# Optimization experiments

Hardware: AMD Instinct MI355X
Metric: run time of the kernel (lower is better)

## Reference

```python
import jax, jax.numpy as jnp
import numpy as np

LAG = 168
HORIZON = 24
D = 6            # d_model = 1 feature + 5-dim position embedding
FF = 18          # dim_feedforward
NL = 3           # num encoder layers
B = 8192
EPS = 1e-5


def setup_inputs() -> dict:
    key = jax.random.key(0)
    ks = jax.random.split(key, 16)
    s = 0.1
    return {
        "input": jax.random.normal(ks[0], (B, LAG), dtype=jnp.float32),
        "pos_emb": jax.random.normal(ks[1], (LAG, 5), dtype=jnp.float32) * s,
        "in_proj_w": jax.random.normal(ks[2], (NL, 3 * D, D), dtype=jnp.float32) * s,
        "in_proj_b": jax.random.normal(ks[3], (NL, 3 * D), dtype=jnp.float32) * s,
        "out_w": jax.random.normal(ks[4], (NL, D, D), dtype=jnp.float32) * s,
        "out_b": jax.random.normal(ks[5], (NL, D), dtype=jnp.float32) * s,
        "ln1_g": jnp.ones((NL, D), dtype=jnp.float32),
        "ln1_b": jnp.zeros((NL, D), dtype=jnp.float32),
        "lin1_w": jax.random.normal(ks[6], (NL, FF, D), dtype=jnp.float32) * s,
        "lin1_b": jax.random.normal(ks[7], (NL, FF), dtype=jnp.float32) * s,
        "lin2_w": jax.random.normal(ks[8], (NL, D, FF), dtype=jnp.float32) * s,
        "lin2_b": jax.random.normal(ks[9], (NL, D), dtype=jnp.float32) * s,
        "ln2_g": jnp.ones((NL, D), dtype=jnp.float32),
        "ln2_b": jnp.zeros((NL, D), dtype=jnp.float32),
        "head_w": jax.random.normal(ks[10], (HORIZON, D * LAG), dtype=jnp.float32) * s,
        "head_b": jax.random.normal(ks[11], (HORIZON,), dtype=jnp.float32) * s,
    }


def _layer_norm(x, g, b):
    m = jnp.mean(x, axis=-1, keepdims=True)
    v = jnp.mean((x - m) ** 2, axis=-1, keepdims=True)
    return (x - m) * jax.lax.rsqrt(v + EPS) * g + b


def reference(input, pos_emb, in_proj_w, in_proj_b, out_w, out_b,
              ln1_g, ln1_b, lin1_w, lin1_b, lin2_w, lin2_b,
              ln2_g, ln2_b, head_w, head_b):
    Bsz, L = input.shape
    # embed positions and concat with raw feature -> [B, L, 6]
    x = jnp.concatenate(
        [input[..., None], jnp.broadcast_to(pos_emb[None], (Bsz, L, 5))], axis=2)

    h = x
    scale = 1.0 / jnp.sqrt(jnp.float32(D))
    for i in range(NL):  # post-norm TransformerEncoderLayer (PyTorch default)
        qkv = jnp.einsum("bld,ed->ble", h, in_proj_w[i]) + in_proj_b[i]  # [B,L,18]
        q, k, v = jnp.split(qkv, 3, axis=-1)  # each [B,L,6], single head
        scores = jnp.einsum("bqd,bkd->bqk", q, k) * scale
        attn = jax.nn.softmax(scores, axis=-1)
        o = jnp.einsum("bqk,bkd->bqd", attn, v)
        o = jnp.einsum("bld,ed->ble", o, out_w[i]) + out_b[i]
        h = _layer_norm(h + o, ln1_g[i], ln1_b[i])
        f = jax.nn.relu(jnp.einsum("bld,fd->blf", h, lin1_w[i]) + lin1_b[i])
        f = jnp.einsum("blf,df->bld", f, lin2_w[i]) + lin2_b[i]
        h = _layer_norm(h + f, ln2_g[i], ln2_b[i])

    h = jax.nn.relu(h + x)              # residual from embedded input + relu
    h = h.reshape(Bsz, L * D)           # flatten
    return h @ head_w.T + head_b        # [B, HORIZON]
```

## Files before the change

kernel.cpp:

```cpp
#include <hip/hip_runtime.h>
#include <math.h>

#define LAG 168
#define HOR 24
#define DM 6
#define FFD 18
#define NL 3
#define LNEPS 1e-5f

typedef unsigned int u32;
typedef float f32x4 __attribute__((ext_vector_type(4)));
typedef float f32x16 __attribute__((ext_vector_type(16)));
typedef short s16x8 __attribute__((ext_vector_type(8)));
typedef __bf16 bfx2 __attribute__((ext_vector_type(2)));

#define VT    0
#define PP    800
#define OOH   2752
#define HEADS 0
#define LDSW  2144

__device__ __forceinline__ u32 pkbf(float a, float b) {
    bfx2 t; t[0] = (__bf16)a; t[1] = (__bf16)b;
    return __builtin_bit_cast(u32, t);
}
__device__ __forceinline__ s16x8 mk8(u32 a, u32 b, u32 c, u32 d) {
    uint4 u; u.x = a; u.y = b; u.z = c; u.w = d;
    return __builtin_bit_cast(s16x8, u);
}
__device__ __forceinline__ float b2f(unsigned short h) {
    u32 u = ((u32)h) << 16; return __builtin_bit_cast(float, u);
}
__device__ __forceinline__ void ln6(const float* r, const float* g, const float* bb, float* outv) {
    float m = (r[0]+r[1]+r[2]+r[3]+r[4]+r[5]) * (1.0f/6.0f);
    float v = 0.f;
#pragma unroll
    for (int d = 0; d < DM; ++d) { float t = r[d]-m; v += t*t; }
    v *= (1.0f/6.0f);
    float rs = __builtin_amdgcn_rsqf(v + LNEPS);
#pragma unroll
    for (int d = 0; d < DM; ++d) outv[d] = (r[d]-m)*rs*g[d] + bb[d];
}

__global__ __launch_bounds__(64, 4) void tfenc_kernel(
    const float* __restrict__ input, const float* __restrict__ pos_emb,
    const float* __restrict__ ipw, const float* __restrict__ ipb,
    const float* __restrict__ ow,  const float* __restrict__ obp,
    const float* __restrict__ l1g, const float* __restrict__ l1b,
    const float* __restrict__ f1w, const float* __restrict__ f1b,
    const float* __restrict__ f2w, const float* __restrict__ f2b,
    const float* __restrict__ l2g, const float* __restrict__ l2b,
    const float* __restrict__ hw,  const float* __restrict__ hb,
    float* __restrict__ out)
{
    __shared__ __align__(16) float lds[LDSW];
    __bf16* ldsh = (__bf16*)lds;
    u32*    ldsu = (u32*)lds;

    const int L = threadIdx.x;
    const int b = blockIdx.x;

    lds[VT + 700 + L] = 0.f;
    if (L < 36) lds[VT + 700 + 64 + L] = 0.f;
    {
        __bf16 one = (__bf16)1.0f;
        ldsh[6*200 + L] = one;
        ldsh[6*200 + 64 + L] = one;
        ldsh[6*200 + 128 + L] = one;
    }

    float hv[3][DM], xv[3][DM];
#pragma unroll
    for (int i = 0; i < 3; ++i) {
        int r = L + 64*i;
        bool real = (r < LAG);
        xv[i][0] = real ? input[(size_t)b*LAG + r] : 0.f;
#pragma unroll
        for (int j = 0; j < 5; ++j)
            xv[i][1+j] = real ? pos_emb[r*5 + j] : 0.f;
#pragma unroll
        for (int d = 0; d < DM; ++d) hv[i][d] = xv[i][d];
    }

    const float cQ = 0.5889116917845058f;
    const u32 himask = (L & 32) ? 0u : ~0u;
    const int permA = 4*(L & 31);
    const int permB = permA + 128;

#pragma unroll 1
    for (int il = 0; il < NL; ++il) {
        const float* Wip = ipw + il*3*DM*DM;
        const float* bip = ipb + il*3*DM;
        const float* Wo  = ow  + il*DM*DM;
        const float* bo  = obp + il*DM;
        const float* g1  = l1g + il*DM;    const float* c1 = l1b + il*DM;
        const float* W1  = f1w + il*FFD*DM; const float* bb1 = f1b + il*FFD;
        const float* W2  = f2w + il*DM*FFD; const float* bb2 = f2b + il*DM;
        const float* g2  = l2g + il*DM;    const float* c2 = l2b + il*DM;

        u32 qp[3][3], kp[3][3];
#pragma unroll
        for (int i = 0; i < 3; ++i) {
            int r = L + 64*i;
            float qv[6], kv[6], vv[6];
#pragma unroll
            for (int e = 0; e < 18; ++e) {
                float a = bip[e];
#pragma unroll
                for (int d = 0; d < DM; ++d) a += hv[i][d]*Wip[e*DM+d];
                if (e < 6) qv[e] = a*cQ;
                else if (e < 12) kv[e-6] = a;
                else vv[e-12] = a;
            }
            qp[i][0]=pkbf(qv[0],qv[1]); qp[i][1]=pkbf(qv[2],qv[3]); qp[i][2]=pkbf(qv[4],qv[5]);
            kp[i][0]=pkbf(kv[0],kv[1]); kp[i][1]=pkbf(kv[2],kv[3]); kp[i][2]=pkbf(kv[4],kv[5]);
#pragma unroll
            for (int d = 0; d < DM; ++d)
                ldsh[d*200 + r] = (__bf16)vv[d];
        }

        s16x8 kf[6];
#pragma unroll
        for (int kt = 0; kt < 6; ++kt) {
            int adr = (kt & 1) ? permB : permA;
            int sl = kt >> 1;
            u32 w0 = ((u32)__builtin_amdgcn_ds_bpermute(adr, (int)kp[sl][0])) & himask;
            u32 w1 = ((u32)__builtin_amdgcn_ds_bpermute(adr, (int)kp[sl][1])) & himask;
            u32 w2 = ((u32)__builtin_amdgcn_ds_bpermute(adr, (int)kp[sl][2])) & himask;
            kf[kt] = mk8(w0, w1, w2, 0u);
        }
        s16x8 vf[6];
        {
            int d = L & 15;
            int vrow = d < 7 ? d : 7;
            const u32* vb = ldsu + (VT + vrow*100 + (L >> 4)*4);
#pragma unroll
            for (int kc = 0; kc < 6; ++kc)
                vf[kc] = __builtin_bit_cast(s16x8, *(const uint4*)(vb + kc*16));
        }

        const int wrbase = PP + (L & 31)*18 + 2*(L >> 5);
        const int rdbase = PP + (L & 15)*18 + 4*(L >> 4);

#pragma unroll
        for (int qt = 0; qt < 6; ++qt) {
            int adr = (qt & 1) ? permB : permA;
            int sl = qt >> 1;
            u32 u0 = ((u32)__builtin_amdgcn_ds_bpermute(adr, (int)qp[sl][0])) & himask;
            u32 u1 = ((u32)__builtin_amdgcn_ds_bpermute(adr, (int)qp[sl][1])) & himask;
            u32 u2 = ((u32)__builtin_amdgcn_ds_bpermute(adr, (int)qp[sl][2])) & himask;
            s16x8 qf = mk8(u0, u1, u2, 0u);
            f32x4 acc0 = {0.f,0.f,0.f,0.f};
            f32x4 acc1 = {0.f,0.f,0.f,0.f};
#pragma unroll
            for (int kt = 0; kt < 6; ++kt) {
                f32x16 z = {};
                f32x16 S = __builtin_amdgcn_mfma_f32_32x32x16_bf16(kf[kt], qf, z, 0, 0, 0);
                u32 w[8];
#pragma unroll
                for (int jj = 0; jj < 8; ++jj) {
                    float pa, pb;
                    if (kt == 5 && jj >= 2) { pa = 0.f; pb = 0.f; }
                    else {
                        pa = __builtin_amdgcn_exp2f(S[2*jj]);
                        pb = __builtin_amdgcn_exp2f(S[2*jj+1]);
                    }
                    w[jj] = pkbf(pa, pb);
                }
                u32* ppw = ldsu + wrbase;
                { uint2 t; t.x=w[0]; t.y=w[1]; *(uint2*)(ppw     ) = t; }
                { uint2 t; t.x=w[2]; t.y=w[3]; *(uint2*)(ppw +  4) = t; }
                { uint2 t; t.x=w[4]; t.y=w[5]; *(uint2*)(ppw +  8) = t; }
                { uint2 t; t.x=w[6]; t.y=w[7]; *(uint2*)(ppw + 12) = t; }
                const u32* rr = ldsu + rdbase;
                uint2 a00 = *(const uint2*)(rr);
                uint2 a01 = *(const uint2*)(rr + 2);
                uint2 a10 = *(const uint2*)(rr + 288);
                uint2 a11 = *(const uint2*)(rr + 290);
                acc0 = __builtin_amdgcn_mfma_f32_16x16x32_bf16(mk8(a00.x,a00.y,a01.x,a01.y), vf[kt], acc0, 0,0,0);
                acc1 = __builtin_amdgcn_mfma_f32_16x16x32_bf16(mk8(a10.x,a10.y,a11.x,a11.y), vf[kt], acc1, 0,0,0);
            }
            int d = L & 15;
            if (d < 7) {
                int qb = 32*qt + 4*(L >> 4);
                __bf16* ob16 = ldsh + OOH;
#pragma unroll
                for (int r2 = 0; r2 < 4; ++r2) {
                    ob16[(qb + r2)*8 + d]      = (__bf16)acc0[r2];
                    ob16[(qb + 16 + r2)*8 + d] = (__bf16)acc1[r2];
                }
            }
        }

#pragma unroll
        for (int i = 0; i < 3; ++i) {
            int r = L + 64*i;
            s16x8 ov = __builtin_bit_cast(s16x8, *(const uint4*)(ldsh + OOH + r*8));
            float o[7];
#pragma unroll
            for (int d = 0; d < 7; ++d) o[d] = b2f((unsigned short)ov[d]);
            float inv = __builtin_amdgcn_rcpf(o[6]);
            float att[6], rv[6];
#pragma unroll
            for (int d = 0; d < 6; ++d) att[d] = o[d]*inv;
#pragma unroll
            for (int e = 0; e < 6; ++e) {
                float a = bo[e];
#pragma unroll
                for (int d = 0; d < 6; ++d) a += att[d]*Wo[e*6+d];
                rv[e] = hv[i][e] + a;
            }
            ln6(rv, g1, c1, hv[i]);
            float o2[6];
#pragma unroll
            for (int d = 0; d < 6; ++d) o2[d] = bb2[d];
#pragma unroll
            for (int ff = 0; ff < FFD; ++ff) {
                float a = bb1[ff];
#pragma unroll
                for (int d = 0; d < 6; ++d) a += hv[i][d]*W1[ff*6+d];
                a = fmaxf(a, 0.f);
#pragma unroll
                for (int d = 0; d < 6; ++d) o2[d] += a*W2[d*FFD+ff];
            }
#pragma unroll
            for (int d = 0; d < 6; ++d) rv[d] = hv[i][d] + o2[d];
            ln6(rv, g2, c2, hv[i]);
        }
    }

    float hf[3][6];
#pragma unroll
    for (int i = 0; i < 3; ++i) {
        int r = L + 64*i;
        bool real = (r < LAG);
#pragma unroll
        for (int d = 0; d < 6; ++d)
            hf[i][d] = real ? fmaxf(hv[i][d] + xv[i][d], 0.f) : 0.f;
    }
    float pt[24];
#pragma unroll
    for (int t = 0; t < 24; ++t) pt[t] = 0.f;
#pragma unroll
    for (int i = 0; i < 3; ++i) {
        int r = L + 64*i;
        if (r < LAG) {
            const float* wr = hw + r*6;
#pragma unroll
            for (int t = 0; t < 24; ++t) {
                const float2* wp = (const float2*)(wr + t*1008);
                float2 w0 = wp[0], w1 = wp[1], w2 = wp[2];
                pt[t] += w0.x*hf[i][0] + w0.y*hf[i][1] + w1.x*hf[i][2]
                       + w1.y*hf[i][3] + w2.x*hf[i][4] + w2.y*hf[i][5];
            }
        }
    }
#pragma unroll
    for (int t = 0; t < 24; ++t) lds[HEADS + L*25 + t] = pt[t];
    if (L < HOR) {
        float s = hb[L];
#pragma unroll 8
        for (int j = 0; j < 64; ++j) s += lds[HEADS + j*25 + L];
        out[(size_t)b*HOR + L] = s;
    }
}

extern "C" void kernel_launch(void* const* d_in, const int* in_sizes, int n_in,
                              void* d_out, int out_size, void* d_ws, size_t ws_size,
                              hipStream_t stream) {
    const float* input   = (const float*)d_in[0];
    const float* pos_emb = (const float*)d_in[1];
    const float* ipw     = (const float*)d_in[2];
    const float* ipb     = (const float*)d_in[3];
    const float* ow      = (const float*)d_in[4];
    const float* ob      = (const float*)d_in[5];
    const float* l1g     = (const float*)d_in[6];
    const float* l1b     = (const float*)d_in[7];
    const float* f1w     = (const float*)d_in[8];
    const float* f1b     = (const float*)d_in[9];
    const float* f2w     = (const float*)d_in[10];
    const float* f2b     = (const float*)d_in[11];
    const float* l2g     = (const float*)d_in[12];
    const float* l2b     = (const float*)d_in[13];
    const float* hw      = (const float*)d_in[14];
    const float* hb      = (const float*)d_in[15];
    float* out = (float*)d_out;

    const int B = in_sizes[0] / LAG;
    tfenc_kernel<<<dim3(B), dim3(64), 0, stream>>>(
        input, pos_emb, ipw, ipb, ow, ob, l1g, l1b,
        f1w, f1b, f2w, f2b, l2g, l2b, hw, hb, out);
}
```

Measured before the change: 172.3 us.

## Pack four samples per block, compact LDS slices, rewrite head as dot products

Each block now runs four independent 64-lane wavefronts, one per batch sample. Each wavefront gets a compact private LDS slice in which the attention-output buffer overlaps the V buffer, and the ones column is rewritten every layer. The aim is to cut block-launch overhead and raise residency (launch bounds become 256 threads, 7 blocks per CU). The output head is also restructured: the activation is staged in LDS, and 48 lanes each compute half of one horizon dot product with float4 loads, combined by a lane shuffle. This replaces the old per-lane 24-output partial sums and LDS cross-lane reduction. It relies on in-wave ordering for the overlapping LDS regions and drops the zero-fill of the padding V row.

```diff
diff --git a/kernel.cpp b/kernel.cpp
--- a/kernel.cpp
+++ b/kernel.cpp
@@ -6,6 +6,7 @@
 #define DM 6
 #define FFD 18
 #define NL 3
+#define WPB 4
 #define LNEPS 1e-5f
 
 typedef unsigned int u32;
@@ -14,11 +15,8 @@
 typedef short s16x8 __attribute__((ext_vector_type(8)));
 typedef __bf16 bfx2 __attribute__((ext_vector_type(2)));
 
-#define VT    0
 #define PP    800
-#define OOH   2752
-#define HEADS 0
-#define LDSW  2144
+#define SLICE 1376
 
 __device__ __forceinline__ u32 pkbf(float a, float b) {
     bfx2 t; t[0] = (__bf16)a; t[1] = (__bf16)b;
@@ -42,7 +40,7 @@
     for (int d = 0; d < DM; ++d) outv[d] = (r[d]-m)*rs*g[d] + bb[d];
 }
 
-__global__ __launch_bounds__(64, 4) void tfenc_kernel(
+__global__ __launch_bounds__(64*WPB, 7) void tfenc_kernel(
     const float* __restrict__ input, const float* __restrict__ pos_emb,
     const float* __restrict__ ipw, const float* __restrict__ ipb,
     const float* __restrict__ ow,  const float* __restrict__ obp,
@@ -53,21 +51,15 @@
     const float* __restrict__ hw,  const float* __restrict__ hb,
     float* __restrict__ out)
 {
-    __shared__ __align__(16) float lds[LDSW];
-    __bf16* ldsh = (__bf16*)lds;
-    u32*    ldsu = (u32*)lds;
-
-    const int L = threadIdx.x;
-    const int b = blockIdx.x;
-
-    lds[VT + 700 + L] = 0.f;
-    if (L < 36) lds[VT + 700 + 64 + L] = 0.f;
-    {
-        __bf16 one = (__bf16)1.0f;
-        ldsh[6*200 + L] = one;
-        ldsh[6*200 + 64 + L] = one;
-        ldsh[6*200 + 128 + L] = one;
-    }
+    __shared__ __align__(16) float lds[WPB * SLICE];
+
+    const int L   = threadIdx.x & 63;
+    const int wid = threadIdx.x >> 6;
+    const int b   = blockIdx.x * WPB + wid;
+
+    float*  sl  = lds + wid * SLICE;
+    __bf16* slh = (__bf16*)sl;
+    u32*    slu = (u32*)sl;
 
     float hv[3][DM], xv[3][DM];
 #pragma unroll
@@ -93,10 +85,10 @@
         const float* bip = ipb + il*3*DM;
         const float* Wo  = ow  + il*DM*DM;
         const float* bo  = obp + il*DM;
-        const float* g1  = l1g + il*DM;    const float* c1 = l1b + il*DM;
+        const float* g1  = l1g + il*DM;     const float* c1  = l1b + il*DM;
         const float* W1  = f1w + il*FFD*DM; const float* bb1 = f1b + il*FFD;
         const float* W2  = f2w + il*DM*FFD; const float* bb2 = f2b + il*DM;
-        const float* g2  = l2g + il*DM;    const float* c2 = l2b + il*DM;
+        const float* g2  = l2g + il*DM;     const float* c2  = l2b + il*DM;
 
         u32 qp[3][3], kp[3][3];
 #pragma unroll
@@ -116,24 +108,30 @@
             kp[i][0]=pkbf(kv[0],kv[1]); kp[i][1]=pkbf(kv[2],kv[3]); kp[i][2]=pkbf(kv[4],kv[5]);
 #pragma unroll
             for (int d = 0; d < DM; ++d)
-                ldsh[d*200 + r] = (__bf16)vv[d];
+                slh[d*200 + r] = (__bf16)vv[d];
+        }
+        {
+            __bf16 one = (__bf16)1.0f;
+            slh[6*200 + L] = one;
+            slh[6*200 + 64 + L] = one;
+            slh[6*200 + 128 + L] = one;
         }
 
         s16x8 kf[6];
 #pragma unroll
         for (int kt = 0; kt < 6; ++kt) {
             int adr = (kt & 1) ? permB : permA;
-            int sl = kt >> 1;
-            u32 w0 = ((u32)__builtin_amdgcn_ds_bpermute(adr, (int)kp[sl][0])) & himask;
-            u32 w1 = ((u32)__builtin_amdgcn_ds_bpermute(adr, (int)kp[sl][1])) & himask;
-            u32 w2 = ((u32)__builtin_amdgcn_ds_bpermute(adr, (int)kp[sl][2])) & himask;
+            int slo = kt >> 1;
+            u32 w0 = ((u32)__builtin_amdgcn_ds_bpermute(adr, (int)kp[slo][0])) & himask;
+            u32 w1 = ((u32)__builtin_amdgcn_ds_bpermute(adr, (int)kp[slo][1])) & himask;
+            u32 w2 = ((u32)__builtin_amdgcn_ds_bpermute(adr, (int)kp[slo][2])) & himask;
             kf[kt] = mk8(w0, w1, w2, 0u);
         }
         s16x8 vf[6];
         {
             int d = L & 15;
             int vrow = d < 7 ? d : 7;
-            const u32* vb = ldsu + (VT + vrow*100 + (L >> 4)*4);
+            const u32* vb = slu + (vrow*100 + (L >> 4)*4);
 #pragma unroll
             for (int kc = 0; kc < 6; ++kc)
                 vf[kc] = __builtin_bit_cast(s16x8, *(const uint4*)(vb + kc*16));
@@ -145,10 +143,10 @@
 #pragma unroll
         for (int qt = 0; qt < 6; ++qt) {
             int adr = (qt & 1) ? permB : permA;
-            int sl = qt >> 1;
-            u32 u0 = ((u32)__builtin_amdgcn_ds_bpermute(adr, (int)qp[sl][0])) & himask;
-            u32 u1 = ((u32)__builtin_amdgcn_ds_bpermute(adr, (int)qp[sl][1])) & himask;
-            u32 u2 = ((u32)__builtin_amdgcn_ds_bpermute(adr, (int)qp[sl][2])) & himask;
+            int slo = qt >> 1;
+            u32 u0 = ((u32)__builtin_amdgcn_ds_bpermute(adr, (int)qp[slo][0])) & himask;
+            u32 u1 = ((u32)__builtin_amdgcn_ds_bpermute(adr, (int)qp[slo][1])) & himask;
+            u32 u2 = ((u32)__builtin_amdgcn_ds_bpermute(adr, (int)qp[slo][2])) & himask;
             s16x8 qf = mk8(u0, u1, u2, 0u);
             f32x4 acc0 = {0.f,0.f,0.f,0.f};
             f32x4 acc1 = {0.f,0.f,0.f,0.f};
@@ -167,12 +165,12 @@
                     }
                     w[jj] = pkbf(pa, pb);
                 }
-                u32* ppw = ldsu + wrbase;
+                u32* ppw = slu + wrbase;
                 { uint2 t; t.x=w[0]; t.y=w[1]; *(uint2*)(ppw     ) = t; }
                 { uint2 t; t.x=w[2]; t.y=w[3]; *(uint2*)(ppw +  4) = t; }
                 { uint2 t; t.x=w[4]; t.y=w[5]; *(uint2*)(ppw +  8) = t; }
                 { uint2 t; t.x=w[6]; t.y=w[7]; *(uint2*)(ppw + 12) = t; }
-                const u32* rr = ldsu + rdbase;
+                const u32* rr = slu + rdbase;
                 uint2 a00 = *(const uint2*)(rr);
                 uint2 a01 = *(const uint2*)(rr + 2);
                 uint2 a10 = *(const uint2*)(rr + 288);
@@ -183,11 +181,10 @@
             int d = L & 15;
             if (d < 7) {
                 int qb = 32*qt + 4*(L >> 4);
-                __bf16* ob16 = ldsh + OOH;
 #pragma unroll
                 for (int r2 = 0; r2 < 4; ++r2) {
-                    ob16[(qb + r2)*8 + d]      = (__bf16)acc0[r2];
-                    ob16[(qb + 16 + r2)*8 + d] = (__bf16)acc1[r2];
+                    slh[(qb + r2)*8 + d]      = (__bf16)acc0[r2];
+                    slh[(qb + 16 + r2)*8 + d] = (__bf16)acc1[r2];
                 }
             }
         }
@@ -195,7 +192,7 @@
 #pragma unroll
         for (int i = 0; i < 3; ++i) {
             int r = L + 64*i;
-            s16x8 ov = __builtin_bit_cast(s16x8, *(const uint4*)(ldsh + OOH + r*8));
+            s16x8 ov = __builtin_bit_cast(s16x8, *(const uint4*)(slh + r*8));
             float o[7];
 #pragma unroll
             for (int d = 0; d < 7; ++d) o[d] = b2f((unsigned short)ov[d]);
@@ -229,39 +226,29 @@
         }
     }
 
-    float hf[3][6];
 #pragma unroll
     for (int i = 0; i < 3; ++i) {
         int r = L + 64*i;
         bool real = (r < LAG);
 #pragma unroll
         for (int d = 0; d < 6; ++d)
-            hf[i][d] = real ? fmaxf(hv[i][d] + xv[i][d], 0.f) : 0.f;
-    }
-    float pt[24];
-#pragma unroll
-    for (int t = 0; t < 24; ++t) pt[t] = 0.f;
-#pragma unroll
-    for (int i = 0; i < 3; ++i) {
-        int r = L + 64*i;
-        if (r < LAG) {
-            const float* wr = hw + r*6;
-#pragma unroll
-            for (int t = 0; t < 24; ++t) {
-                const float2* wp = (const float2*)(wr + t*1008);
-                float2 w0 = wp[0], w1 = wp[1], w2 = wp[2];
-                pt[t] += w0.x*hf[i][0] + w0.y*hf[i][1] + w1.x*hf[i][2]
-                       + w1.y*hf[i][3] + w2.x*hf[i][4] + w2.y*hf[i][5];
-            }
-        }
-    }
-#pragma unroll
-    for (int t = 0; t < 24; ++t) lds[HEADS + L*25 + t] = pt[t];
-    if (L < HOR) {
-        float s = hb[L];
-#pragma unroll 8
-        for (int j = 0; j < 64; ++j) s += lds[HEADS + j*25 + L];
-        out[(size_t)b*HOR + L] = s;
+            sl[r*6 + d] = real ? fmaxf(hv[i][d] + xv[i][d], 0.f) : 0.f;
+    }
+    {
+        int t = L >> 1, half = L & 1;
+        float p = 0.f;
+        if (L < 48) {
+            const float4* wv  = (const float4*)(hw + (size_t)t*1008 + half*504);
+            const float4* hv4 = (const float4*)(sl + half*504);
+#pragma unroll 6
+            for (int k = 0; k < 126; ++k) {
+                float4 w = wv[k], h = hv4[k];
+                p += w.x*h.x + w.y*h.y + w.z*h.z + w.w*h.w;
+            }
+        }
+        p += __shfl_xor(p, 1);
+        if (L < 48 && half == 0)
+            out[(size_t)b*HOR + t] = p + hb[t];
     }
 }
 
@@ -287,7 +274,7 @@
     float* out = (float*)d_out;
 
     const int B = in_sizes[0] / LAG;
-    tfenc_kernel<<<dim3(B), dim3(64), 0, stream>>>(
+    tfenc_kernel<<<dim3(B / WPB), dim3(64 * WPB), 0, stream>>>(
         input, pos_emb, ipw, ipb, ow, ob, l1g, l1b,
         f1w, f1b, f2w, f2b, l2g, l2b, hw, hb, out);
 }
```

Result: slower. 379.8 us (+120.5%).
